# Kernel tuning notes

Measured on AMD Instinct MI355X. Metric: run time of the kernel, lower is better.

Reference implementation:

```python
import jax, jax.numpy as jnp
import numpy as np

N, G, E, H, Z = 50000, 2000, 800000, 512, 64
BN_EPS = 1e-5


def setup_inputs() -> dict:
    key = jax.random.key(0)
    ks = jax.random.split(key, 10)
    x = jax.random.normal(ks[0], (N, G), dtype=jnp.float32)
    edge_index = jax.random.randint(ks[1], (2, E), 0, N, dtype=jnp.int32)
    s1 = 1.0 / np.sqrt(G)
    s2 = 1.0 / np.sqrt(H)
    return {
        "x": x,
        "edge_index": edge_index,
        "W1l": jax.random.normal(ks[2], (G, H), dtype=jnp.float32) * s1,
        "b1": jnp.zeros((H,), jnp.float32),
        "W1r": jax.random.normal(ks[3], (G, H), dtype=jnp.float32) * s1,
        "bn_gamma": jax.random.uniform(ks[4], (H,), dtype=jnp.float32) + 0.5,
        "bn_beta": jax.random.normal(ks[5], (H,), dtype=jnp.float32) * 0.1,
        "bn_mean": jax.random.normal(ks[6], (H,), dtype=jnp.float32) * 0.1,
        "bn_var": jax.random.uniform(ks[7], (H,), dtype=jnp.float32) + 0.5,
        "W2l": jax.random.normal(ks[8], (H, Z), dtype=jnp.float32) * s2,
        "b2": jnp.zeros((Z,), jnp.float32),
        "W2r": jax.random.normal(ks[9], (H, Z), dtype=jnp.float32) * s2,
    }


def _sage_conv(h, src, dst, Wl, bl, Wr, n_nodes):
    # mean aggregation of source features at destination nodes
    msg = h[src]  # [E, D] gather
    agg = jax.ops.segment_sum(msg, dst, num_segments=n_nodes)
    cnt = jax.ops.segment_sum(jnp.ones((src.shape[0],), h.dtype), dst, num_segments=n_nodes)
    agg = agg / jnp.maximum(cnt, 1.0)[:, None]
    # PyG SAGEConv: lin_l(agg) + lin_r(x), bias only on lin_l
    return agg @ Wl + bl + h @ Wr


def reference(x, edge_index, W1l, b1, W1r, bn_gamma, bn_beta, bn_mean, bn_var, W2l, b2, W2r):
    src, dst = edge_index[0], edge_index[1]
    n = x.shape[0]
    h = _sage_conv(x, src, dst, W1l, b1, W1r, n)  # [N, H]
    # BatchNorm1d (eval mode: running stats) + ReLU; dropout is identity at inference
    h = (h - bn_mean) * (bn_gamma / jnp.sqrt(bn_var + BN_EPS)) + bn_beta
    h = jax.nn.relu(h)
    z = _sage_conv(h, src, dst, W2l, b2, W2r, n)  # [N, Z]
    return z
```

## Files before the change

kernel.cpp:

```cpp
#include <hip/hip_runtime.h>


#define BN_EPS 1e-5f
#define GK 2000
#define KP 2048
#define NT1C 63
#define NT1P 64
#define NT2 16

typedef __attribute__((ext_vector_type(8))) short bf16x8;
typedef __attribute__((ext_vector_type(4))) float f32x4;
typedef unsigned short u16x8 __attribute__((ext_vector_type(8)));

__device__ inline unsigned short f2bf(float f) {
    union { float f; unsigned u; } v; v.f = f;
    unsigned r = (v.u + 0x7fffu + ((v.u >> 16) & 1u)) >> 16;
    return (unsigned short)r;
}
__device__ inline float bf2f(unsigned short u) {
    union { unsigned u; float f; } v; v.u = ((unsigned)u) << 16;
    return v.f;
}

#define GLL16(gp, lp) __builtin_amdgcn_global_load_lds( \
    (const __attribute__((address_space(1))) void*)(gp), \
    (__attribute__((address_space(3))) void*)(lp), 16, 0, 0)

__global__ __launch_bounds__(256) void prep_fused(
    const float* __restrict__ x, unsigned short* __restrict__ xb,
    const float* __restrict__ W1l, const float* __restrict__ W1r,
    const float* __restrict__ gamma, const float* __restrict__ beta,
    const float* __restrict__ mean, const float* __restrict__ var,
    const float* __restrict__ b1, unsigned short* __restrict__ BT,
    const float* __restrict__ W2l, const float* __restrict__ W2r,
    unsigned short* __restrict__ BT2, float* __restrict__ b1p,
    const int* __restrict__ ei, int* __restrict__ cnt, int N, int E)
{
    const int bb = blockIdx.x;
    if (bb < 2048) {
        const int total8 = N * 256;
        for (int idx = bb * 256 + threadIdx.x; idx < total8; idx += 2048 * 256) {
            int row = idx >> 8;
            int k8  = idx & 255;
            unsigned short us[8];
            if (k8 < 250) {
                const float4* p = (const float4*)(x + (size_t)row * 2000 + k8 * 8);
                float4 v0 = p[0], v1 = p[1];
                us[0]=f2bf(v0.x); us[1]=f2bf(v0.y); us[2]=f2bf(v0.z); us[3]=f2bf(v0.w);
                us[4]=f2bf(v1.x); us[5]=f2bf(v1.y); us[6]=f2bf(v1.z); us[7]=f2bf(v1.w);
            } else {
#pragma unroll
                for (int j = 0; j < 8; ++j) us[j] = 0;
            }
            *(u16x8*)&xb[(size_t)row * 2048 + k8 * 8] = *(u16x8*)us;
        }
    } else if (bb < 3072) {
        int idx = (bb - 2048) * 256 + threadIdx.x;
        int c  = idx >> 8;
        int k0 = (idx & 255) << 3;
        int cc = (c < 512) ? c : c - 512;
        float scv = gamma[cc] * rsqrtf(var[cc] + BN_EPS);
        const float* W = (c < 512) ? (W1l + cc) : (W1r + cc);
        unsigned short us[8];
#pragma unroll
        for (int j = 0; j < 8; ++j) {
            int k = k0 + j;
            float v = (k < GK) ? W[(size_t)k * 512] * scv : 0.0f;
            us[j] = f2bf(v);
        }
        *(u16x8*)&BT[(size_t)c * KP + k0] = *(u16x8*)us;
    } else if (bb < 3104) {
        int idx = (bb - 3072) * 256 + threadIdx.x;
        int c  = idx >> 6;
        int k0 = (idx & 63) << 3;
        const float* W = (c < 64) ? (W2l + c) : (W2r + (c - 64));
        unsigned short us[8];
#pragma unroll
        for (int j = 0; j < 8; ++j) us[j] = f2bf(W[(size_t)(k0 + j) * 64]);
        *(u16x8*)&BT2[(size_t)c * 512 + k0] = *(u16x8*)us;
    } else if (bb == 3104) {
#pragma unroll
        for (int h = 0; h < 2; ++h) {
            int c = threadIdx.x + h * 256;
            float scv = gamma[c] * rsqrtf(var[c] + BN_EPS);
            b1p[c] = b1[c] * scv + (beta[c] - mean[c] * scv);
        }
    } else {
        for (int i = (bb - 3105) * 256 + threadIdx.x; i < E; i += 991 * 256)
            atomicAdd(&cnt[ei[E + i]], 1);
    }
}

__global__ __launch_bounds__(1024) void scan_kernel(const int* __restrict__ cnt,
                                                    int* __restrict__ row_start, int n) {
    __shared__ int part[1024];
    int t = threadIdx.x;
    int chunk = (n + 1023) >> 10;
    int lo = t * chunk;
    int hi = lo + chunk; if (hi > n) hi = n;
    int s = 0;
    for (int i = lo; i < hi; ++i) s += cnt[i];
    part[t] = s;
    __syncthreads();
    for (int off = 1; off < 1024; off <<= 1) {
        int add = (t >= off) ? part[t - off] : 0;
        __syncthreads();
        part[t] += add;
        __syncthreads();
    }
    int run = (t == 0) ? 0 : part[t - 1];
    for (int i = lo; i < hi; ++i) { row_start[i] = run; run += cnt[i]; }
    if (t == 1023) row_start[n] = part[1023];
}

__global__ void fill_kernel(const int* __restrict__ ei, int E,
                            const int* __restrict__ row_start,
                            int* __restrict__ cnt, int* __restrict__ colidx) {
    int i = blockIdx.x * blockDim.x + threadIdx.x;
    if (i < E) {
        int d = ei[E + i];
        int p = atomicSub(&cnt[d], 1) - 1;
        colidx[row_start[d] + p] = ei[i];
    }
}

__global__ __launch_bounds__(512) void gemm1_256(
    const unsigned short* __restrict__ xb, int M,
    const unsigned short* __restrict__ BT,
    unsigned short* __restrict__ Y)
{
    __shared__ __align__(16) unsigned short As[3][8192];
    __shared__ __align__(16) unsigned short Bs[3][8192];

    const int t = threadIdx.x, wid = t >> 6, lane = t & 63;
    const int nbr = (M + 255) >> 8;
    const int nwg = nbr * 4;
    const int b   = blockIdx.x;
    int swz;
    if ((nwg & 7) == 0) swz = (b & 7) * (nwg >> 3) + (b >> 3);
    else swz = b;
    const int row0 = (swz >> 2) << 8;
    const int col0 = (swz & 3) << 8;

    const int c0 = t, c1 = t + 512;
    const int g0 = ((c0 & 3) ^ ((c0 >> 3) & 3)) << 3;
    const int g1 = ((c1 & 3) ^ ((c1 >> 3) & 3)) << 3;
    int ra0 = row0 + (c0 >> 2); if (ra0 >= M) ra0 = M - 1;
    int ra1 = row0 + (c1 >> 2); if (ra1 >= M) ra1 = M - 1;
    const unsigned short* aS0 = xb + (size_t)ra0 * KP + g0;
    const unsigned short* aS1 = xb + (size_t)ra1 * KP + g1;
    const unsigned short* bS0 = BT + (size_t)(col0 + (c0 >> 2)) * KP + g0;
    const unsigned short* bS1 = BT + (size_t)(col0 + (c1 >> 2)) * KP + g1;

    const int wr = wid >> 2, wc = wid & 3;
    const int fr16 = lane & 15;
    const int gswr = ((lane >> 4) ^ ((fr16 >> 1) & 3)) << 4;

    f32x4 acc[8][4];
#pragma unroll
    for (int m = 0; m < 8; ++m)
#pragma unroll
        for (int n = 0; n < 4; ++n) acc[m][n] = (f32x4)0.0f;

#define STG(kt, buf) do {                                          \
        unsigned short* ab_ = &As[buf][0];                         \
        unsigned short* bb_ = &Bs[buf][0];                         \
        GLL16(aS0 + (size_t)(kt) * 32, ab_ + c0 * 8);              \
        GLL16(aS1 + (size_t)(kt) * 32, ab_ + c1 * 8);              \
        GLL16(bS0 + (size_t)(kt) * 32, bb_ + c0 * 8);              \
        GLL16(bS1 + (size_t)(kt) * 32, bb_ + c1 * 8);              \
    } while (0)

    STG(0, 0);
    STG(1, 1);

    int rb = 0;
    for (int it = 0; it < NT1P; ++it) {
        if (it == NT1P - 1) {
            asm volatile("s_waitcnt vmcnt(0)" ::: "memory");
        } else {
            asm volatile("s_waitcnt vmcnt(4)" ::: "memory");
        }
        __builtin_amdgcn_s_barrier();
        __builtin_amdgcn_sched_barrier(0);

        const char* Ab = (const char*)&As[rb][0];
        const char* Bb = (const char*)&Bs[rb][0];
        bf16x8 af[8], bfr[4];
#pragma unroll
        for (int m = 0; m < 8; ++m)
            af[m] = *(const bf16x8*)(Ab + ((wr * 128 + m * 16 + fr16) << 6) + gswr);
#pragma unroll
        for (int n = 0; n < 4; ++n)
            bfr[n] = *(const bf16x8*)(Bb + ((wc * 64 + n * 16 + fr16) << 6) + gswr);

        if (it + 2 < NT1P) {
            int wb = rb + 2; if (wb >= 3) wb -= 3;
            STG(it + 2, wb);
        }

        __builtin_amdgcn_s_setprio(1);
#pragma unroll
        for (int m = 0; m < 8; ++m)
#pragma unroll
            for (int n = 0; n < 4; ++n)
                acc[m][n] = __builtin_amdgcn_mfma_f32_16x16x32_bf16(
                    af[m], bfr[n], acc[m][n], 0, 0, 0);
        __builtin_amdgcn_s_setprio(0);

        rb = (rb == 2) ? 0 : rb + 1;
    }
#undef STG

    const int crow = (lane >> 4) << 2;
#pragma unroll
    for (int m = 0; m < 8; ++m) {
        int rbase = row0 + wr * 128 + m * 16 + crow;
#pragma unroll
        for (int r = 0; r < 4; ++r) {
            int row = rbase + r;
            if (row < M) {
                unsigned short* Yp = Y + (size_t)row * 1024 + col0 + wc * 64 + fr16;
#pragma unroll
                for (int n = 0; n < 4; ++n)
                    Yp[n * 16] = f2bf(acc[m][n][r]);
            }
        }
    }
}

__global__ __launch_bounds__(256) void gemm1_cvt(
    const float* __restrict__ A, int M,
    const unsigned short* __restrict__ BT,
    unsigned short* __restrict__ Y)
{
    __shared__ __align__(16) unsigned short As[128][32];
    __shared__ __align__(16) unsigned short Bs[2][128][32];

    const int t    = threadIdx.x;
    const int wid  = t >> 6;
    const int lane = t & 63;
    const int nby = (M + 127) >> 7;
    const int b   = blockIdx.x;
    const int swz = (b & 7) * nby + (b >> 3);
    const int row0 = (swz >> 3) << 7;
    const int col0 = (swz & 7) << 7;

    const int ar  = t >> 1;
    const int akq = (t & 1) << 4;
    int garow = row0 + ar; if (garow >= M) garow = M - 1;
    const float* aptr = A + (size_t)garow * GK + akq;

    const int i0 = wid * 64 + lane;
    const unsigned short* bptr0 = BT + ((size_t)(col0 + (i0 >> 2)) * KP + ((i0 & 3) << 3));
    const unsigned short* bptr1 = bptr0 + (size_t)64 * KP;

    const int wr   = wid >> 1, wc = wid & 1;
    const int fr16 = lane & 15;
    const int kb8  = (lane >> 4) << 3;

    f32x4 acc[4][4];
#pragma unroll
    for (int m = 0; m < 4; ++m)
#pragma unroll
        for (int n = 0; n < 4; ++n) acc[m][n] = (f32x4)0.0f;

    GLL16(bptr0, &Bs[0][wid * 16][0]);
    GLL16(bptr1, &Bs[0][64 + wid * 16][0]);

    float frg[16];
    {
        const float4* p = (const float4*)aptr;
        float4 v0 = p[0], v1 = p[1], v2 = p[2], v3 = p[3];
        frg[0]=v0.x; frg[1]=v0.y; frg[2]=v0.z;  frg[3]=v0.w;
        frg[4]=v1.x; frg[5]=v1.y; frg[6]=v1.z;  frg[7]=v1.w;
        frg[8]=v2.x; frg[9]=v2.y; frg[10]=v2.z; frg[11]=v2.w;
        frg[12]=v3.x;frg[13]=v3.y;frg[14]=v3.z; frg[15]=v3.w;
    }

    int cur = 0;
    for (int it = 0; it < NT1C; ++it) {
        {
            unsigned short us[16];
#pragma unroll
            for (int j = 0; j < 16; ++j) us[j] = f2bf(frg[j]);
            *(u16x8*)&As[ar][akq]     = *(u16x8*)&us[0];
            *(u16x8*)&As[ar][akq + 8] = *(u16x8*)&us[8];
        }
        __syncthreads();

        if (it + 1 < NT1C) {
            int kb = (it + 1) * 32 + akq;
            if (kb < GK) {
                const float4* p = (const float4*)(aptr + (size_t)(it + 1) * 32);
                float4 v0 = p[0], v1 = p[1], v2 = p[2], v3 = p[3];
                frg[0]=v0.x; frg[1]=v0.y; frg[2]=v0.z;  frg[3]=v0.w;
                frg[4]=v1.x; frg[5]=v1.y; frg[6]=v1.z;  frg[7]=v1.w;
                frg[8]=v2.x; frg[9]=v2.y; frg[10]=v2.z; frg[11]=v2.w;
                frg[12]=v3.x;frg[13]=v3.y;frg[14]=v3.z; frg[15]=v3.w;
            } else {
#pragma unroll
                for (int j = 0; j < 16; ++j) frg[j] = 0.0f;
            }
            const unsigned short* bp = bptr0 + (size_t)(it + 1) * 32;
            GLL16(bp,                   &Bs[cur ^ 1][wid * 16][0]);
            GLL16(bp + (size_t)64 * KP, &Bs[cur ^ 1][64 + wid * 16][0]);
        }

        bf16x8 af[4], bfr[4];
#pragma unroll
        for (int m = 0; m < 4; ++m)
            af[m] = *(const bf16x8*)&As[wr * 64 + m * 16 + fr16][kb8];
#pragma unroll
        for (int n = 0; n < 4; ++n)
            bfr[n] = *(const bf16x8*)&Bs[cur][wc * 64 + n * 16 + fr16][kb8];
#pragma unroll
        for (int m = 0; m < 4; ++m)
#pragma unroll
            for (int n = 0; n < 4; ++n)
                acc[m][n] = __builtin_amdgcn_mfma_f32_16x16x32_bf16(
                    af[m], bfr[n], acc[m][n], 0, 0, 0);

        __syncthreads();
        cur ^= 1;
    }

    const int crow = (lane >> 4) << 2;
#pragma unroll
    for (int m = 0; m < 4; ++m) {
        int rbase = row0 + wr * 64 + m * 16 + crow;
#pragma unroll
        for (int r = 0; r < 4; ++r) {
            int row = rbase + r;
            if (row < M) {
                unsigned short* Yp = Y + (size_t)row * 1024 + col0 + wc * 64 + fr16;
#pragma unroll
                for (int n = 0; n < 4; ++n)
                    Yp[n * 16] = f2bf(acc[m][n][r]);
            }
        }
    }
}

__global__ __launch_bounds__(256) void agg1_kernel(
    const unsigned short* __restrict__ Y, unsigned short* __restrict__ Hh,
    const int* __restrict__ row_start, const int* __restrict__ colidx,
    const float* __restrict__ b1p, int n)
{
    int wid  = (blockIdx.x * blockDim.x + threadIdx.x) >> 6;
    int lane = threadIdx.x & 63;
    if (wid >= n) return;
    int c0 = lane * 8;
    float bb[8];
    *(float4*)&bb[0] = *(const float4*)&b1p[c0];
    *(float4*)&bb[4] = *(const float4*)&b1p[c0 + 4];

    int s0 = row_start[wid], s1 = row_start[wid + 1];
    float acc[8] = {0, 0, 0, 0, 0, 0, 0, 0};
    int i = s0;
    for (; i + 2 <= s1; i += 2) {
        int src0 = colidx[i], src1 = colidx[i + 1];
        u16x8 v0 = *(const u16x8*)&Y[(size_t)src0 * 1024 + c0];
        u16x8 v1 = *(const u16x8*)&Y[(size_t)src1 * 1024 + c0];
#pragma unroll
        for (int j = 0; j < 8; ++j) acc[j] += bf2f(v0[j]) + bf2f(v1[j]);
    }
    if (i < s1) {
        int src = colidx[i];
        u16x8 v = *(const u16x8*)&Y[(size_t)src * 1024 + c0];
#pragma unroll
        for (int j = 0; j < 8; ++j) acc[j] += bf2f(v[j]);
    }
    float inv = 1.0f / fmaxf((float)(s1 - s0), 1.0f);
    u16x8 sv = *(const u16x8*)&Y[(size_t)wid * 1024 + 512 + c0];
    unsigned short o[8];
#pragma unroll
    for (int j = 0; j < 8; ++j) {
        float pre = acc[j] * inv + bb[j] + bf2f(sv[j]);
        o[j] = f2bf(fmaxf(pre, 0.0f));
    }
    *(u16x8*)&Hh[(size_t)wid * 512 + c0] = *(u16x8*)o;
}

__global__ __launch_bounds__(256) void gemm2_bf16(
    const unsigned short* __restrict__ Hh, int M,
    const unsigned short* __restrict__ BT2,
    unsigned short* __restrict__ U)
{
    __shared__ __align__(16) unsigned short As[2][128][32];
    __shared__ __align__(16) unsigned short Bs[2][128][32];

    const int t    = threadIdx.x;
    const int wid  = t >> 6;
    const int lane = t & 63;
    const int row0 = blockIdx.x << 7;

    const int c_lo = wid * 64 + lane;
    const int c_hi = c_lo + 256;
    const int s_lo = ((c_lo & 3) ^ ((c_lo >> 3) & 3)) << 3;
    const int s_hi = ((c_hi & 3) ^ ((c_hi >> 3) & 3)) << 3;
    int ra = row0 + (c_lo >> 2); if (ra >= M) ra = M - 1;
    int rbw = row0 + (c_hi >> 2); if (rbw >= M) rbw = M - 1;
    const unsigned short* aSrc0 = Hh + (size_t)ra * 512 + s_lo;
    const unsigned short* aSrc1 = Hh + (size_t)rbw * 512 + s_hi;
    const unsigned short* bSrc0 = BT2 + (size_t)(c_lo >> 2) * 512 + s_lo;
    const unsigned short* bSrc1 = BT2 + (size_t)(c_hi >> 2) * 512 + s_hi;

    const int wr   = wid >> 1, wc = wid & 1;
    const int fr16 = lane & 15;
    const int gsw2 = ((lane >> 4) ^ ((fr16 >> 1) & 3)) << 4;

    f32x4 acc[4][4];
#pragma unroll
    for (int m = 0; m < 4; ++m)
#pragma unroll
        for (int n = 0; n < 4; ++n) acc[m][n] = (f32x4)0.0f;

#define STAGE2(kt, buf) do {                                                  \
        int ko = (kt) * 32;                                                   \
        GLL16(aSrc0 + ko, (unsigned short*)&As[buf][0][0] + (size_t)c_lo * 8);  \
        GLL16(aSrc1 + ko, (unsigned short*)&As[buf][0][0] + (size_t)c_hi * 8);  \
        GLL16(bSrc0 + ko, (unsigned short*)&Bs[buf][0][0] + (size_t)c_lo * 8);  \
        GLL16(bSrc1 + ko, (unsigned short*)&Bs[buf][0][0] + (size_t)c_hi * 8);  \
    } while (0)

    STAGE2(0, 0);
    int cur = 0;
    for (int it = 0; it < NT2; ++it) {
        __syncthreads();
        if (it + 1 < NT2) STAGE2(it + 1, cur ^ 1);

        const char* Ab = (const char*)&As[cur][0][0];
        const char* Bb = (const char*)&Bs[cur][0][0];
        bf16x8 af[4], bfr[4];
#pragma unroll
        for (int m = 0; m < 4; ++m)
            af[m] = *(const bf16x8*)(Ab + ((wr * 64 + m * 16 + fr16) << 6) + gsw2);
#pragma unroll
        for (int n = 0; n < 4; ++n)
            bfr[n] = *(const bf16x8*)(Bb + ((wc * 64 + n * 16 + fr16) << 6) + gsw2);
#pragma unroll
        for (int m = 0; m < 4; ++m)
#pragma unroll
            for (int n = 0; n < 4; ++n)
                acc[m][n] = __builtin_amdgcn_mfma_f32_16x16x32_bf16(
                    af[m], bfr[n], acc[m][n], 0, 0, 0);
        cur ^= 1;
    }
#undef STAGE2

    const int crow = (lane >> 4) << 2;
#pragma unroll
    for (int m = 0; m < 4; ++m) {
        int rbase = row0 + wr * 64 + m * 16 + crow;
#pragma unroll
        for (int r = 0; r < 4; ++r) {
            int row = rbase + r;
            if (row < M) {
                unsigned short* Up = U + (size_t)row * 128 + wc * 64 + fr16;
#pragma unroll
                for (int n = 0; n < 4; ++n)
                    Up[n * 16] = f2bf(acc[m][n][r]);
            }
        }
    }
}

__global__ __launch_bounds__(256) void agg2_kernel(
    const unsigned short* __restrict__ U,
    const int* __restrict__ row_start, const int* __restrict__ colidx,
    const float* __restrict__ b2, float* __restrict__ out, int n)
{
    int wid  = (blockIdx.x * blockDim.x + threadIdx.x) >> 6;
    int lane = threadIdx.x & 63;
    if (wid >= n) return;
    int s0 = row_start[wid], s1 = row_start[wid + 1];
    float acc = 0.f;
    int i = s0;
    for (; i + 2 <= s1; i += 2) {
        int src0 = colidx[i], src1 = colidx[i + 1];
        acc += bf2f(U[(size_t)src0 * 128 + lane]) + bf2f(U[(size_t)src1 * 128 + lane]);
    }
    if (i < s1) acc += bf2f(U[(size_t)colidx[i] * 128 + lane]);
    float inv = 1.0f / fmaxf((float)(s1 - s0), 1.0f);
    float z = acc * inv + b2[lane] + bf2f(U[(size_t)wid * 128 + 64 + lane]);
    out[(size_t)wid * 64 + lane] = z;
}

extern "C" void kernel_launch(void* const* d_in, const int* in_sizes, int n_in,
                              void* d_out, int out_size, void* d_ws, size_t ws_size,
                              hipStream_t stream) {
    const float* x     = (const float*)d_in[0];
    const int*   ei    = (const int*)d_in[1];
    const float* W1l   = (const float*)d_in[2];
    const float* b1    = (const float*)d_in[3];
    const float* W1r   = (const float*)d_in[4];
    const float* gamma = (const float*)d_in[5];
    const float* beta  = (const float*)d_in[6];
    const float* mean  = (const float*)d_in[7];
    const float* var   = (const float*)d_in[8];
    const float* W2l   = (const float*)d_in[9];
    const float* b2    = (const float*)d_in[10];
    const float* W2r   = (const float*)d_in[11];
    float* out = (float*)d_out;

    const int N = in_sizes[0] / 2000;
    const int E = in_sizes[1] / 2;
    const int nby = (N + 127) / 128;

    char* ws = (char*)d_ws;

    size_t need = (size_t)N * KP * 2 + (size_t)N * 1024 * 2
                + (size_t)1024 * KP * 2 + (size_t)128 * 512 * 2 + 2048
                + ((size_t)2 * N + 8 + (size_t)E) * 4;

    if (ws_size >= need) {
        unsigned short* xb  = (unsigned short*)ws;
        unsigned short* Y   = xb + (size_t)N * KP;
        unsigned short* BT  = Y + (size_t)N * 1024;
        unsigned short* BT2 = BT + (size_t)1024 * KP;
        float* b1p     = (float*)(BT2 + (size_t)128 * 512);
        int* cnt       = (int*)(b1p + 512);
        int* row_start = cnt + N;
        int* colidx    = row_start + N + 4;
        unsigned short* Hh = xb;
        unsigned short* U  = Y;

        hipMemsetAsync(cnt, 0, (size_t)N * sizeof(int), stream);

        prep_fused<<<4096, 256, 0, stream>>>(
            x, xb, W1l, W1r, gamma, beta, mean, var, b1, BT,
            W2l, W2r, BT2, b1p, ei, cnt, N, E);

        scan_kernel<<<1, 1024, 0, stream>>>(cnt, row_start, N);
        int eb = (E + 255) / 256;
        fill_kernel<<<eb, 256, 0, stream>>>(ei, E, row_start, cnt, colidx);

        int nbr = (N + 255) / 256;
        gemm1_256<<<nbr * 4, 512, 0, stream>>>(xb, N, BT, Y);
        agg1_kernel<<<(N + 3) / 4, 256, 0, stream>>>(
            Y, Hh, row_start, colidx, b1p, N);
        gemm2_bf16<<<nby, 256, 0, stream>>>(Hh, N, BT2, U);
        agg2_kernel<<<(N + 3) / 4, 256, 0, stream>>>(
            U, row_start, colidx, b2, out, N);
    } else {
        unsigned short* Y   = (unsigned short*)ws;
        unsigned short* Hh  = Y + (size_t)N * 1024;
        unsigned short* U   = Hh + (size_t)N * 512;
        unsigned short* BT  = U + (size_t)N * 128;
        unsigned short* BT2 = BT + (size_t)1024 * KP;
        float* b1p     = (float*)(BT2 + (size_t)128 * 512);
        int* cnt       = (int*)(b1p + 512);
        int* row_start = cnt + N;
        int* colidx    = row_start + N + 4;

        hipMemsetAsync(cnt, 0, (size_t)N * sizeof(int), stream);

        prep_fused<<<2048, 256, 0, stream>>>(
            x, (unsigned short*)Y , W1l, W1r, gamma, beta, mean, var,
            b1, BT, W2l, W2r, BT2, b1p, ei, cnt, 0, 0);
        prep_fused<<<4096, 256, 0, stream>>>(
            x, (unsigned short*)Y, W1l, W1r, gamma, beta, mean, var,
            b1, BT, W2l, W2r, BT2, b1p, ei, cnt, 0, E);

        scan_kernel<<<1, 1024, 0, stream>>>(cnt, row_start, N);
        int eb = (E + 255) / 256;
        fill_kernel<<<eb, 256, 0, stream>>>(ei, E, row_start, cnt, colidx);

        gemm1_cvt<<<8 * nby, 256, 0, stream>>>(x, N, BT, Y);
        agg1_kernel<<<(N + 3) / 4, 256, 0, stream>>>(
            Y, Hh, row_start, colidx, b1p, N);
        gemm2_bf16<<<nby, 256, 0, stream>>>(Hh, N, BT2, U);
        agg2_kernel<<<(N + 3) / 4, 256, 0, stream>>>(
            U, row_start, colidx, b2, out, N);
    }
}
```

Before: 701.2 us.

## Fuse fp32-to-bf16 conversion of x into the 256x256 GEMM1 A-tile load

Removes the separate pass that converted x to a padded bf16 buffer. The 256x256 GEMM1 kernel now loads fp32 x into registers two stages ahead, converts to bf16 and writes A tiles to LDS, while B still uses direct global-to-LDS loads. This saves a full write and re-read of a 200MB bf16 copy of x. In exchange the GEMM doubles its A-side global traffic, adds register pressure and conversion ALU work, and uses clamped offsets for the K tail instead of zero padding. The workspace-size fallback path and gemm1_cvt are removed.

```diff
diff --git a/kernel.cpp b/kernel.cpp
--- a/kernel.cpp
+++ b/kernel.cpp
@@ -4,8 +4,7 @@
 #define BN_EPS 1e-5f
 #define GK 2000
 #define KP 2048
-#define NT1C 63
-#define NT1P 64
+#define NT1 63
 #define NT2 16
 
 typedef __attribute__((ext_vector_type(8))) short bf16x8;
@@ -27,35 +26,17 @@
     (__attribute__((address_space(3))) void*)(lp), 16, 0, 0)
 
 __global__ __launch_bounds__(256) void prep_fused(
-    const float* __restrict__ x, unsigned short* __restrict__ xb,
     const float* __restrict__ W1l, const float* __restrict__ W1r,
     const float* __restrict__ gamma, const float* __restrict__ beta,
     const float* __restrict__ mean, const float* __restrict__ var,
     const float* __restrict__ b1, unsigned short* __restrict__ BT,
     const float* __restrict__ W2l, const float* __restrict__ W2r,
     unsigned short* __restrict__ BT2, float* __restrict__ b1p,
-    const int* __restrict__ ei, int* __restrict__ cnt, int N, int E)
+    const int* __restrict__ ei, int* __restrict__ cnt, int E)
 {
     const int bb = blockIdx.x;
-    if (bb < 2048) {
-        const int total8 = N * 256;
-        for (int idx = bb * 256 + threadIdx.x; idx < total8; idx += 2048 * 256) {
-            int row = idx >> 8;
-            int k8  = idx & 255;
-            unsigned short us[8];
-            if (k8 < 250) {
-                const float4* p = (const float4*)(x + (size_t)row * 2000 + k8 * 8);
-                float4 v0 = p[0], v1 = p[1];
-                us[0]=f2bf(v0.x); us[1]=f2bf(v0.y); us[2]=f2bf(v0.z); us[3]=f2bf(v0.w);
-                us[4]=f2bf(v1.x); us[5]=f2bf(v1.y); us[6]=f2bf(v1.z); us[7]=f2bf(v1.w);
-            } else {
-#pragma unroll
-                for (int j = 0; j < 8; ++j) us[j] = 0;
-            }
-            *(u16x8*)&xb[(size_t)row * 2048 + k8 * 8] = *(u16x8*)us;
-        }
-    } else if (bb < 3072) {
-        int idx = (bb - 2048) * 256 + threadIdx.x;
+    if (bb < 1024) {
+        int idx = bb * 256 + threadIdx.x;
         int c  = idx >> 8;
         int k0 = (idx & 255) << 3;
         int cc = (c < 512) ? c : c - 512;
@@ -69,8 +50,8 @@
             us[j] = f2bf(v);
         }
         *(u16x8*)&BT[(size_t)c * KP + k0] = *(u16x8*)us;
-    } else if (bb < 3104) {
-        int idx = (bb - 3072) * 256 + threadIdx.x;
+    } else if (bb < 1056) {
+        int idx = (bb - 1024) * 256 + threadIdx.x;
         int c  = idx >> 6;
         int k0 = (idx & 63) << 3;
         const float* W = (c < 64) ? (W2l + c) : (W2r + (c - 64));
@@ -78,7 +59,7 @@
 #pragma unroll
         for (int j = 0; j < 8; ++j) us[j] = f2bf(W[(size_t)(k0 + j) * 64]);
         *(u16x8*)&BT2[(size_t)c * 512 + k0] = *(u16x8*)us;
-    } else if (bb == 3104) {
+    } else if (bb == 1056) {
 #pragma unroll
         for (int h = 0; h < 2; ++h) {
             int c = threadIdx.x + h * 256;
@@ -86,7 +67,7 @@
             b1p[c] = b1[c] * scv + (beta[c] - mean[c] * scv);
         }
     } else {
-        for (int i = (bb - 3105) * 256 + threadIdx.x; i < E; i += 991 * 256)
+        for (int i = (bb - 1057) * 256 + threadIdx.x; i < E; i += 1024 * 256)
             atomicAdd(&cnt[ei[E + i]], 1);
     }
 }
@@ -125,7 +106,7 @@
 }
 
 __global__ __launch_bounds__(512) void gemm1_256(
-    const unsigned short* __restrict__ xb, int M,
+    const float* __restrict__ x, int M,
     const unsigned short* __restrict__ BT,
     unsigned short* __restrict__ Y)
 {
@@ -143,14 +124,16 @@
     const int col0 = (swz & 3) << 8;
 
     const int c0 = t, c1 = t + 512;
-    const int g0 = ((c0 & 3) ^ ((c0 >> 3) & 3)) << 3;
-    const int g1 = ((c1 & 3) ^ ((c1 >> 3) & 3)) << 3;
+    const int gf0 = ((c0 & 3) ^ ((c0 >> 3) & 3)) << 3;
+    const int gf1 = ((c1 & 3) ^ ((c1 >> 3) & 3)) << 3;
     int ra0 = row0 + (c0 >> 2); if (ra0 >= M) ra0 = M - 1;
     int ra1 = row0 + (c1 >> 2); if (ra1 >= M) ra1 = M - 1;
-    const unsigned short* aS0 = xb + (size_t)ra0 * KP + g0;
-    const unsigned short* aS1 = xb + (size_t)ra1 * KP + g1;
-    const unsigned short* bS0 = BT + (size_t)(col0 + (c0 >> 2)) * KP + g0;
-    const unsigned short* bS1 = BT + (size_t)(col0 + (c1 >> 2)) * KP + g1;
+    const float* aR0 = x + (size_t)ra0 * GK + gf0;
+    const float* aR1 = x + (size_t)ra1 * GK + gf1;
+    const int omax0 = 1992 - gf0;
+    const int omax1 = 1992 - gf1;
+    const unsigned short* bS0 = BT + (size_t)(col0 + (c0 >> 2)) * KP + (gf0);
+    const unsigned short* bS1 = BT + (size_t)(col0 + (c1 >> 2)) * KP + (gf1);
 
     const int wr = wid >> 2, wc = wid & 3;
     const int fr16 = lane & 15;
@@ -162,25 +145,48 @@
 #pragma unroll
         for (int n = 0; n < 4; ++n) acc[m][n] = (f32x4)0.0f;
 
-#define STG(kt, buf) do {                                          \
-        unsigned short* ab_ = &As[buf][0];                         \
-        unsigned short* bb_ = &Bs[buf][0];                         \
-        GLL16(aS0 + (size_t)(kt) * 32, ab_ + c0 * 8);              \
-        GLL16(aS1 + (size_t)(kt) * 32, ab_ + c1 * 8);              \
-        GLL16(bS0 + (size_t)(kt) * 32, bb_ + c0 * 8);              \
-        GLL16(bS1 + (size_t)(kt) * 32, bb_ + c1 * 8);              \
+    float sa[16], sb[16];
+
+#define LOADA(st, kt) do {                                                \
+        int o0 = (kt) * 32; if (o0 > omax0) o0 = omax0;                   \
+        int o1 = (kt) * 32; if (o1 > omax1) o1 = omax1;                   \
+        const float4* p0 = (const float4*)(aR0 + o0);                     \
+        const float4* p1 = (const float4*)(aR1 + o1);                     \
+        float4 u0 = p0[0], u1 = p0[1], u2 = p1[0], u3 = p1[1];            \
+        st[0]=u0.x; st[1]=u0.y; st[2]=u0.z;  st[3]=u0.w;                  \
+        st[4]=u1.x; st[5]=u1.y; st[6]=u1.z;  st[7]=u1.w;                  \
+        st[8]=u2.x; st[9]=u2.y; st[10]=u2.z; st[11]=u2.w;                 \
+        st[12]=u3.x; st[13]=u3.y; st[14]=u3.z; st[15]=u3.w;               \
     } while (0)
 
-    STG(0, 0);
-    STG(1, 1);
+#define CVTW(st, buf) do {                                                \
+        unsigned short us_[16];                                           \
+        _Pragma("unroll")                                                 \
+        for (int j_ = 0; j_ < 16; ++j_) us_[j_] = f2bf(st[j_]);           \
+        unsigned short* ab_ = &As[buf][0];                                \
+        *(u16x8*)(ab_ + c0 * 8) = *(u16x8*)&us_[0];                       \
+        *(u16x8*)(ab_ + c1 * 8) = *(u16x8*)&us_[8];                       \
+    } while (0)
+
+#define STGB(kt, buf) do {                                                \
+        unsigned short* bb_ = &Bs[buf][0];                                \
+        GLL16(bS0 + (size_t)(kt) * 32, bb_ + c0 * 8);                     \
+        GLL16(bS1 + (size_t)(kt) * 32, bb_ + c1 * 8);                     \
+    } while (0)
+
+    LOADA(sa, 0); STGB(0, 0);
+    LOADA(sb, 1); STGB(1, 1);
 
     int rb = 0;
-    for (int it = 0; it < NT1P; ++it) {
-        if (it == NT1P - 1) {
+    for (int it = 0; it < NT1; ++it) {
+        if ((it & 1) == 0) CVTW(sa, rb); else CVTW(sb, rb);
+
+        if (it == NT1 - 1) {
             asm volatile("s_waitcnt vmcnt(0)" ::: "memory");
         } else {
-            asm volatile("s_waitcnt vmcnt(4)" ::: "memory");
-        }
+            asm volatile("s_waitcnt vmcnt(6)" ::: "memory");
+        }
+        asm volatile("s_waitcnt lgkmcnt(0)" ::: "memory");
         __builtin_amdgcn_s_barrier();
         __builtin_amdgcn_sched_barrier(0);
 
@@ -194,9 +200,10 @@
         for (int n = 0; n < 4; ++n)
             bfr[n] = *(const bf16x8*)(Bb + ((wc * 64 + n * 16 + fr16) << 6) + gswr);
 
-        if (it + 2 < NT1P) {
+        if (it + 2 < NT1) {
             int wb = rb + 2; if (wb >= 3) wb -= 3;
-            STG(it + 2, wb);
+            if ((it & 1) == 0) LOADA(sa, it + 2); else LOADA(sb, it + 2);
+            STGB(it + 2, wb);
         }
 
         __builtin_amdgcn_s_setprio(1);
@@ -210,125 +217,14 @@
 
         rb = (rb == 2) ? 0 : rb + 1;
     }
-#undef STG
+#undef LOADA
+#undef CVTW
+#undef STGB
 
     const int crow = (lane >> 4) << 2;
 #pragma unroll
     for (int m = 0; m < 8; ++m) {
         int rbase = row0 + wr * 128 + m * 16 + crow;
-#pragma unroll
-        for (int r = 0; r < 4; ++r) {
-            int row = rbase + r;
-            if (row < M) {
-                unsigned short* Yp = Y + (size_t)row * 1024 + col0 + wc * 64 + fr16;
-#pragma unroll
-                for (int n = 0; n < 4; ++n)
-                    Yp[n * 16] = f2bf(acc[m][n][r]);
-            }
-        }
-    }
-}
-
-__global__ __launch_bounds__(256) void gemm1_cvt(
-    const float* __restrict__ A, int M,
-    const unsigned short* __restrict__ BT,
-    unsigned short* __restrict__ Y)
-{
-    __shared__ __align__(16) unsigned short As[128][32];
-    __shared__ __align__(16) unsigned short Bs[2][128][32];
-
-    const int t    = threadIdx.x;
-    const int wid  = t >> 6;
-    const int lane = t & 63;
-    const int nby = (M + 127) >> 7;
-    const int b   = blockIdx.x;
-    const int swz = (b & 7) * nby + (b >> 3);
-    const int row0 = (swz >> 3) << 7;
-    const int col0 = (swz & 7) << 7;
-
-    const int ar  = t >> 1;
-    const int akq = (t & 1) << 4;
-    int garow = row0 + ar; if (garow >= M) garow = M - 1;
-    const float* aptr = A + (size_t)garow * GK + akq;
-
-    const int i0 = wid * 64 + lane;
-    const unsigned short* bptr0 = BT + ((size_t)(col0 + (i0 >> 2)) * KP + ((i0 & 3) << 3));
-    const unsigned short* bptr1 = bptr0 + (size_t)64 * KP;
-
-    const int wr   = wid >> 1, wc = wid & 1;
-    const int fr16 = lane & 15;
-    const int kb8  = (lane >> 4) << 3;
-
-    f32x4 acc[4][4];
-#pragma unroll
-    for (int m = 0; m < 4; ++m)
-#pragma unroll
-        for (int n = 0; n < 4; ++n) acc[m][n] = (f32x4)0.0f;
-
-    GLL16(bptr0, &Bs[0][wid * 16][0]);
-    GLL16(bptr1, &Bs[0][64 + wid * 16][0]);
-
-    float frg[16];
-    {
-        const float4* p = (const float4*)aptr;
-        float4 v0 = p[0], v1 = p[1], v2 = p[2], v3 = p[3];
-        frg[0]=v0.x; frg[1]=v0.y; frg[2]=v0.z;  frg[3]=v0.w;
-        frg[4]=v1.x; frg[5]=v1.y; frg[6]=v1.z;  frg[7]=v1.w;
-        frg[8]=v2.x; frg[9]=v2.y; frg[10]=v2.z; frg[11]=v2.w;
-        frg[12]=v3.x;frg[13]=v3.y;frg[14]=v3.z; frg[15]=v3.w;
-    }
-
-    int cur = 0;
-    for (int it = 0; it < NT1C; ++it) {
-        {
-            unsigned short us[16];
-#pragma unroll
-            for (int j = 0; j < 16; ++j) us[j] = f2bf(frg[j]);
-            *(u16x8*)&As[ar][akq]     = *(u16x8*)&us[0];
-            *(u16x8*)&As[ar][akq + 8] = *(u16x8*)&us[8];
-        }
-        __syncthreads();
-
-        if (it + 1 < NT1C) {
-            int kb = (it + 1) * 32 + akq;
-            if (kb < GK) {
-                const float4* p = (const float4*)(aptr + (size_t)(it + 1) * 32);
-                float4 v0 = p[0], v1 = p[1], v2 = p[2], v3 = p[3];
-                frg[0]=v0.x; frg[1]=v0.y; frg[2]=v0.z;  frg[3]=v0.w;
-                frg[4]=v1.x; frg[5]=v1.y; frg[6]=v1.z;  frg[7]=v1.w;
-                frg[8]=v2.x; frg[9]=v2.y; frg[10]=v2.z; frg[11]=v2.w;
-                frg[12]=v3.x;frg[13]=v3.y;frg[14]=v3.z; frg[15]=v3.w;
-            } else {
-#pragma unroll
-                for (int j = 0; j < 16; ++j) frg[j] = 0.0f;
-            }
-            const unsigned short* bp = bptr0 + (size_t)(it + 1) * 32;
-            GLL16(bp,                   &Bs[cur ^ 1][wid * 16][0]);
-            GLL16(bp + (size_t)64 * KP, &Bs[cur ^ 1][64 + wid * 16][0]);
-        }
-
-        bf16x8 af[4], bfr[4];
-#pragma unroll
-        for (int m = 0; m < 4; ++m)
-            af[m] = *(const bf16x8*)&As[wr * 64 + m * 16 + fr16][kb8];
-#pragma unroll
-        for (int n = 0; n < 4; ++n)
-            bfr[n] = *(const bf16x8*)&Bs[cur][wc * 64 + n * 16 + fr16][kb8];
-#pragma unroll
-        for (int m = 0; m < 4; ++m)
-#pragma unroll
-            for (int n = 0; n < 4; ++n)
-                acc[m][n] = __builtin_amdgcn_mfma_f32_16x16x32_bf16(
-                    af[m], bfr[n], acc[m][n], 0, 0, 0);
-
-        __syncthreads();
-        cur ^= 1;
-    }
-
-    const int crow = (lane >> 4) << 2;
-#pragma unroll
-    for (int m = 0; m < 4; ++m) {
-        int rbase = row0 + wr * 64 + m * 16 + crow;
 #pragma unroll
         for (int r = 0; r < 4; ++r) {
             int row = rbase + r;
@@ -509,69 +405,31 @@
     const int nby = (N + 127) / 128;
 
     char* ws = (char*)d_ws;
-
-    size_t need = (size_t)N * KP * 2 + (size_t)N * 1024 * 2
-                + (size_t)1024 * KP * 2 + (size_t)128 * 512 * 2 + 2048
-                + ((size_t)2 * N + 8 + (size_t)E) * 4;
-
-    if (ws_size >= need) {
-        unsigned short* xb  = (unsigned short*)ws;
-        unsigned short* Y   = xb + (size_t)N * KP;
-        unsigned short* BT  = Y + (size_t)N * 1024;
-        unsigned short* BT2 = BT + (size_t)1024 * KP;
-        float* b1p     = (float*)(BT2 + (size_t)128 * 512);
-        int* cnt       = (int*)(b1p + 512);
-        int* row_start = cnt + N;
-        int* colidx    = row_start + N + 4;
-        unsigned short* Hh = xb;
-        unsigned short* U  = Y;
-
-        hipMemsetAsync(cnt, 0, (size_t)N * sizeof(int), stream);
-
-        prep_fused<<<4096, 256, 0, stream>>>(
-            x, xb, W1l, W1r, gamma, beta, mean, var, b1, BT,
-            W2l, W2r, BT2, b1p, ei, cnt, N, E);
-
-        scan_kernel<<<1, 1024, 0, stream>>>(cnt, row_start, N);
-        int eb = (E + 255) / 256;
-        fill_kernel<<<eb, 256, 0, stream>>>(ei, E, row_start, cnt, colidx);
-
-        int nbr = (N + 255) / 256;
-        gemm1_256<<<nbr * 4, 512, 0, stream>>>(xb, N, BT, Y);
-        agg1_kernel<<<(N + 3) / 4, 256, 0, stream>>>(
-            Y, Hh, row_start, colidx, b1p, N);
-        gemm2_bf16<<<nby, 256, 0, stream>>>(Hh, N, BT2, U);
-        agg2_kernel<<<(N + 3) / 4, 256, 0, stream>>>(
-            U, row_start, colidx, b2, out, N);
-    } else {
-        unsigned short* Y   = (unsigned short*)ws;
-        unsigned short* Hh  = Y + (size_t)N * 1024;
-        unsigned short* U   = Hh + (size_t)N * 512;
-        unsigned short* BT  = U + (size_t)N * 128;
-        unsigned short* BT2 = BT + (size_t)1024 * KP;
-        float* b1p     = (float*)(BT2 + (size_t)128 * 512);
-        int* cnt       = (int*)(b1p + 512);
-        int* row_start = cnt + N;
-        int* colidx    = row_start + N + 4;
-
-        hipMemsetAsync(cnt, 0, (size_t)N * sizeof(int), stream);
-
-        prep_fused<<<2048, 256, 0, stream>>>(
-            x, (unsigned short*)Y , W1l, W1r, gamma, beta, mean, var,
-            b1, BT, W2l, W2r, BT2, b1p, ei, cnt, 0, 0);
-        prep_fused<<<4096, 256, 0, stream>>>(
-            x, (unsigned short*)Y, W1l, W1r, gamma, beta, mean, var,
-            b1, BT, W2l, W2r, BT2, b1p, ei, cnt, 0, E);
-
-        scan_kernel<<<1, 1024, 0, stream>>>(cnt, row_start, N);
-        int eb = (E + 255) / 256;
-        fill_kernel<<<eb, 256, 0, stream>>>(ei, E, row_start, cnt, colidx);
-
-        gemm1_cvt<<<8 * nby, 256, 0, stream>>>(x, N, BT, Y);
-        agg1_kernel<<<(N + 3) / 4, 256, 0, stream>>>(
-            Y, Hh, row_start, colidx, b1p, N);
-        gemm2_bf16<<<nby, 256, 0, stream>>>(Hh, N, BT2, U);
-        agg2_kernel<<<(N + 3) / 4, 256, 0, stream>>>(
-            U, row_start, colidx, b2, out, N);
-    }
-}
+    unsigned short* Y   = (unsigned short*)ws;
+    unsigned short* Hh  = Y + (size_t)N * 1024;
+    unsigned short* BT  = Hh + (size_t)N * 512;
+    unsigned short* BT2 = BT + (size_t)1024 * KP;
+    float* b1p     = (float*)(BT2 + (size_t)128 * 512);
+    int* cnt       = (int*)(b1p + 512);
+    int* row_start = cnt + N;
+    int* colidx    = row_start + N + 4;
+    unsigned short* U = Y;
+
+    hipMemsetAsync(cnt, 0, (size_t)N * sizeof(int), stream);
+
+    prep_fused<<<2081, 256, 0, stream>>>(
+        W1l, W1r, gamma, beta, mean, var, b1, BT, W2l, W2r, BT2, b1p,
+        ei, cnt, E);
+
+    scan_kernel<<<1, 1024, 0, stream>>>(cnt, row_start, N);
+    int eb = (E + 255) / 256;
+    fill_kernel<<<eb, 256, 0, stream>>>(ei, E, row_start, cnt, colidx);
+
+    int nbr = (N + 255) / 256;
+    gemm1_256<<<nbr * 4, 512, 0, stream>>>(x, N, BT, Y);
+    agg1_kernel<<<(N + 3) / 4, 256, 0, stream>>>(
+        Y, Hh, row_start, colidx, b1p, N);
+    gemm2_bf16<<<nby, 256, 0, stream>>>(Hh, N, BT2, U);
+    agg2_kernel<<<(N + 3) / 4, 256, 0, stream>>>(
+        U, row_start, colidx, b2, out, N);
+}
```

Result: slower. 926.6 us (+32.1%).
